# Optimization experiments

Hardware: AMD Instinct MI355X
Metric: run time of the kernel (lower is better)

The kernel has to match this reference:

```python
import jax, jax.numpy as jnp
import numpy as np

D = 384      # embedding_dim (module-level global)
H = 6        # num_heads
HD = D // H  # head_size = 64
T = 256      # block_size (tril buffer cap)
B = 128


def _layernorm(x, gamma, beta, eps=1e-5):
    mu = jnp.mean(x, axis=-1, keepdims=True)
    var = jnp.var(x, axis=-1, keepdims=True)
    return (x - mu) * jax.lax.rsqrt(var + eps) * gamma + beta


def setup_inputs() -> dict:
    key = jax.random.key(0)
    ks = jax.random.split(key, 12)
    s = 0.02
    return {
        "x":   jax.random.normal(ks[0], (B, T, D), jnp.float32),
        "Wq":  jax.random.normal(ks[1], (H, D, HD), jnp.float32) * s,
        "Wk":  jax.random.normal(ks[2], (H, D, HD), jnp.float32) * s,
        "Wv":  jax.random.normal(ks[3], (H, D, HD), jnp.float32) * s,
        "Wp":  jax.random.normal(ks[4], (D, D), jnp.float32) * s,
        "bp":  jnp.zeros((D,), jnp.float32),
        "W1":  jax.random.normal(ks[5], (D, 4 * D), jnp.float32) * s,
        "b1":  jnp.zeros((4 * D,), jnp.float32),
        "W2":  jax.random.normal(ks[6], (4 * D, D), jnp.float32) * s,
        "b2":  jnp.zeros((D,), jnp.float32),
        "g1":  jnp.ones((D,), jnp.float32),
        "be1": jnp.zeros((D,), jnp.float32),
        "g2":  jnp.ones((D,), jnp.float32),
        "be2": jnp.zeros((D,), jnp.float32),
    }


def reference(x, Wq, Wk, Wv, Wp, bp, W1, b1, W2, b2, g1, be1, g2, be2):
    Bsz, Tlen, C = x.shape
    # pre-LN self-attention
    h = _layernorm(x, g1, be1)
    q = jnp.einsum("btd,hdk->bhtk", h, Wq)
    k = jnp.einsum("bsd,hdk->bhsk", h, Wk)
    v = jnp.einsum("bsd,hdk->bhsk", h, Wv)
    # NOTE: source divides by sqrt(C)=sqrt(embedding_dim), not sqrt(head_size)
    scores = jnp.einsum("bhtk,bhsk->bhts", q, k) / jnp.sqrt(jnp.float32(C))
    causal = jnp.tril(jnp.ones((Tlen, Tlen), bool))
    scores = jnp.where(causal, scores, jnp.float32(-jnp.inf))
    attn = jax.nn.softmax(scores, axis=-1)          # dropout = identity (eval)
    o = jnp.einsum("bhts,bhsk->bhtk", attn, v)      # [B,H,T,HD]
    o = o.transpose(0, 2, 1, 3).reshape(Bsz, Tlen, C)  # concat heads
    sa = o @ Wp + bp
    x = x + sa
    # pre-LN feed-forward
    h2 = _layernorm(x, g2, be2)
    ff = jax.nn.relu(h2 @ W1 + b1) @ W2 + b2
    return x + ff
```

## Files before the change

kernel.cpp:

```cpp
#include <hip/hip_runtime.h>
#include <cstdint>
#include <cstddef>

#define D_   384
#define Hn   6
#define HDm  64
#define T_   256
#define B_   128
#define NROW (B_ * T_)

typedef __bf16  bf16x8 __attribute__((ext_vector_type(8)));
typedef float   f32x4  __attribute__((ext_vector_type(4)));
typedef const __attribute__((address_space(1))) void gvoid;
typedef __attribute__((address_space(3))) void lvoid;

__device__ inline uint32_t bf16rn(float f) {
  uint32_t u = __float_as_uint(f);
  return (u + 0x7FFFu + ((u >> 16) & 1u)) >> 16;
}

__global__ __launch_bounds__(128) void ln_kernel(const float* __restrict__ x,
                                                 const float* __restrict__ g,
                                                 const float* __restrict__ b,
                                                 uint16_t* __restrict__ out) {
  int row = blockIdx.x, tid = threadIdx.x;
  const float* xr = x + (size_t)row * D_;
  float v0 = xr[tid], v1 = xr[tid + 128], v2 = xr[tid + 256];
  float s  = v0 + v1 + v2;
  float ss = v0 * v0 + v1 * v1 + v2 * v2;
#pragma unroll
  for (int off = 32; off > 0; off >>= 1) {
    s  += __shfl_down(s, off);
    ss += __shfl_down(ss, off);
  }
  __shared__ float red[4];
  if ((tid & 63) == 0) { red[(tid >> 6) * 2] = s; red[(tid >> 6) * 2 + 1] = ss; }
  __syncthreads();
  float S = red[0] + red[2], SS = red[1] + red[3];
  float mu  = S * (1.0f / D_);
  float var = SS * (1.0f / D_) - mu * mu;
  float inv = rsqrtf(var + 1e-5f);
  uint16_t* orow = out + (size_t)row * D_;
  orow[tid]       = (uint16_t)bf16rn((v0 - mu) * inv * g[tid]       + b[tid]);
  orow[tid + 128] = (uint16_t)bf16rn((v1 - mu) * inv * g[tid + 128] + b[tid + 128]);
  orow[tid + 256] = (uint16_t)bf16rn((v2 - mu) * inv * g[tid + 256] + b[tid + 256]);
}

__global__ __launch_bounds__(256) void pack_qkv_w(const float* __restrict__ Wq,
                                                  const float* __restrict__ Wk,
                                                  const float* __restrict__ Wv,
                                                  uint16_t* __restrict__ Wo) {
  int idx = blockIdx.x * 256 + threadIdx.x;
  if (idx >= 1152 * D_) return;
  int col = idx / D_, d = idx % D_;
  int which = col / 384, c2 = col % 384;
  int h = c2 / HDm, k = c2 % HDm;
  const float* W = (which == 0) ? Wq : (which == 1) ? Wk : Wv;
  Wo[idx] = (uint16_t)bf16rn(W[((size_t)h * D_ + d) * HDm + k]);
}

__global__ __launch_bounds__(256) void pack_wt(const float* __restrict__ W,
                                               uint16_t* __restrict__ Wt,
                                               int K, int N) {
  int idx = blockIdx.x * 256 + threadIdx.x;
  if (idx >= K * N) return;
  int n = idx / K, k = idx % K;
  Wt[idx] = (uint16_t)bf16rn(W[(size_t)k * N + n]);
}

__global__ __launch_bounds__(256) void gemm_bf16(const uint16_t* __restrict__ A,
                                                 const uint16_t* __restrict__ Bt,
                                                 const float* __restrict__ bias,
                                                 const float* __restrict__ resid,
                                                 void* __restrict__ Cout,
                                                 int M, int N, int K,
                                                 int relu, int store_f32) {
  __shared__ uint16_t As[128 * 32];
  __shared__ uint16_t Bs[128 * 32];
  int tid = threadIdx.x;
  int bm = blockIdx.x * 128, bn = blockIdx.y * 128;
  int lane = tid & 63, wave = tid >> 6;
  int wm = (wave >> 1) << 6;
  int wn = (wave & 1) << 6;
  int lr = lane & 15;
  int q  = lane >> 4;
  int r0 = q << 2;
  int rd_off = (q ^ (lr & 3)) << 3;

  f32x4 acc[4][4];
  const f32x4 zero = {0.f, 0.f, 0.f, 0.f};
#pragma unroll
  for (int i = 0; i < 4; ++i)
#pragma unroll
    for (int j = 0; j < 4; ++j) acc[i][j] = zero;

  for (int k0 = 0; k0 < K; k0 += 32) {
    __syncthreads();
#pragma unroll
    for (int t = 0; t < 2; ++t) {
      int c = t * 256 + tid;
      int row = c >> 2, cc = c & 3;
      int gc = cc ^ (row & 3);
      const uint16_t* ga = A  + (size_t)(bm + row) * K + (k0 + gc * 8);
      const uint16_t* gb = Bt + (size_t)(bn + row) * K + (k0 + gc * 8);
      __builtin_amdgcn_global_load_lds((gvoid*)ga, (lvoid*)((char*)As + c * 16), 16, 0, 0);
      __builtin_amdgcn_global_load_lds((gvoid*)gb, (lvoid*)((char*)Bs + c * 16), 16, 0, 0);
    }
    __syncthreads();

    bf16x8 af[4], bfr[4];
#pragma unroll
    for (int i = 0; i < 4; ++i)
      af[i] = *(const bf16x8*)&As[(wm + i * 16 + lr) * 32 + rd_off];
#pragma unroll
    for (int j = 0; j < 4; ++j)
      bfr[j] = *(const bf16x8*)&Bs[(wn + j * 16 + lr) * 32 + rd_off];
#pragma unroll
    for (int i = 0; i < 4; ++i)
#pragma unroll
      for (int j = 0; j < 4; ++j)
        acc[i][j] = __builtin_amdgcn_mfma_f32_16x16x32_bf16(af[i], bfr[j], acc[i][j], 0, 0, 0);
  }

#pragma unroll
  for (int i = 0; i < 4; ++i) {
#pragma unroll
    for (int r = 0; r < 4; ++r) {
      int rr = bm + wm + i * 16 + r0 + r;
#pragma unroll
      for (int j = 0; j < 4; ++j) {
        int col = bn + wn + j * 16 + lr;
        float v = acc[i][j][r];
        if (bias)  v += bias[col];
        if (relu)  v = fmaxf(v, 0.0f);
        if (resid) v += resid[(size_t)rr * N + col];
        if (store_f32) ((float*)Cout)[(size_t)rr * N + col] = v;
        else           ((uint16_t*)Cout)[(size_t)rr * N + col] = (uint16_t)bf16rn(v);
      }
    }
  }
}

__global__ __launch_bounds__(256, 2) void attn_mfma(const uint16_t* __restrict__ qkv,
                                                    uint16_t* __restrict__ o) {
  __shared__ uint16_t Kt[64 * 72];
  __shared__ uint16_t Vt[64 * 72];
  __shared__ uint16_t Pb[4 * 64 * 72];
  int bh = blockIdx.x;
  int b = bh / Hn, h = bh % Hn;
  int tid = threadIdx.x;
  int lane = tid & 63, w = tid >> 6;
  int ln = lane & 15, q = lane >> 4;
  int kq = q * 8;
  int m0 = w * 64;
  const uint16_t* base = qkv + (size_t)b * T_ * 1152;

  bf16x8 af[4][2];
#pragma unroll
  for (int i = 0; i < 4; ++i)
#pragma unroll
    for (int ks = 0; ks < 2; ++ks)
      af[i][ks] = *(const bf16x8*)(base + (size_t)(m0 + i * 16 + ln) * 1152 + h * HDm + ks * 32 + kq);

  f32x4 o_[4][4], m_[4], l_[4];
  const f32x4 zero = {0.f, 0.f, 0.f, 0.f};
#pragma unroll
  for (int i = 0; i < 4; ++i) {
    m_[i] = {-1e30f, -1e30f, -1e30f, -1e30f};
    l_[i] = zero;
#pragma unroll
    for (int n = 0; n < 4; ++n) o_[i][n] = zero;
  }
  const float cs = 0.07362222f;

  for (int jt = 0; jt < 4; ++jt) {
    if (jt) __syncthreads();
#pragma unroll
    for (int t = 0; t < 2; ++t) {
      int c = t * 256 + tid;
      int s = c >> 3, d0 = (c & 7) << 3;
      *(uint4*)&Kt[s * 72 + d0] =
          *(const uint4*)(base + (size_t)(jt * 64 + s) * 1152 + 384 + h * HDm + d0);
    }
    {
      int sv = tid & 63, dv = (tid >> 6) << 4;
      const uint16_t* gv = base + (size_t)(jt * 64 + sv) * 1152 + 768 + h * HDm + dv;
      uint16_t tmp[16];
      *(uint4*)&tmp[0] = *(const uint4*)gv;
      *(uint4*)&tmp[8] = *(const uint4*)(gv + 8);
#pragma unroll
      for (int jj = 0; jj < 16; ++jj) Vt[(dv + jj) * 72 + sv] = tmp[jj];
    }
    __syncthreads();

    if (w >= jt) {
      f32x4 s2[4][4];
#pragma unroll
      for (int i = 0; i < 4; ++i)
#pragma unroll
        for (int j = 0; j < 4; ++j) s2[i][j] = zero;
#pragma unroll
      for (int ks = 0; ks < 2; ++ks) {
        bf16x8 bf[4];
#pragma unroll
        for (int j = 0; j < 4; ++j)
          bf[j] = *(const bf16x8*)&Kt[(j * 16 + ln) * 72 + ks * 32 + kq];
#pragma unroll
        for (int i = 0; i < 4; ++i)
#pragma unroll
          for (int j = 0; j < 4; ++j)
            s2[i][j] = __builtin_amdgcn_mfma_f32_16x16x32_bf16(af[i][ks], bf[j], s2[i][j], 0, 0, 0);
      }
#pragma unroll
      for (int i = 0; i < 4; ++i) {
#pragma unroll
        for (int j = 0; j < 4; ++j)
#pragma unroll
          for (int r = 0; r < 4; ++r) s2[i][j][r] *= cs;
        if (jt == w) {
#pragma unroll
          for (int j = 0; j < 4; ++j)
#pragma unroll
            for (int r = 0; r < 4; ++r)
              if (j * 16 + ln > i * 16 + q * 4 + r) s2[i][j][r] = -1e30f;
        }
        f32x4 rm;
#pragma unroll
        for (int r = 0; r < 4; ++r)
          rm[r] = fmaxf(fmaxf(s2[i][0][r], s2[i][1][r]), fmaxf(s2[i][2][r], s2[i][3][r]));
#pragma unroll
        for (int off = 1; off < 16; off <<= 1)
#pragma unroll
          for (int r = 0; r < 4; ++r)
            rm[r] = fmaxf(rm[r], __shfl_xor(rm[r], off));
        f32x4 mn, al, ps;
#pragma unroll
        for (int r = 0; r < 4; ++r) {
          mn[r] = fmaxf(m_[i][r], rm[r]);
          al[r] = exp2f(m_[i][r] - mn[r]);
          ps[r] = 0.f;
        }
        m_[i] = mn;
#pragma unroll
        for (int j = 0; j < 4; ++j)
#pragma unroll
          for (int r = 0; r < 4; ++r) {
            float p = exp2f(s2[i][j][r] - mn[r]);
            s2[i][j][r] = p;
            ps[r] += p;
          }
#pragma unroll
        for (int r = 0; r < 4; ++r) l_[i][r] = l_[i][r] * al[r] + ps[r];
#pragma unroll
        for (int n = 0; n < 4; ++n)
#pragma unroll
          for (int r = 0; r < 4; ++r) o_[i][n][r] *= al[r];
#pragma unroll
        for (int j = 0; j < 4; ++j)
#pragma unroll
          for (int r = 0; r < 4; ++r)
            Pb[w * 4608 + (i * 16 + q * 4 + r) * 72 + j * 16 + ln] =
                (uint16_t)bf16rn(s2[i][j][r]);
      }
      bf16x8 pa[4][2];
#pragma unroll
      for (int i = 0; i < 4; ++i)
#pragma unroll
        for (int ks = 0; ks < 2; ++ks)
          pa[i][ks] = *(const bf16x8*)&Pb[w * 4608 + (i * 16 + ln) * 72 + ks * 32 + kq];
#pragma unroll
      for (int n = 0; n < 4; ++n) {
        bf16x8 bv0 = *(const bf16x8*)&Vt[(n * 16 + ln) * 72 + kq];
        bf16x8 bv1 = *(const bf16x8*)&Vt[(n * 16 + ln) * 72 + 32 + kq];
#pragma unroll
        for (int i = 0; i < 4; ++i) {
          o_[i][n] = __builtin_amdgcn_mfma_f32_16x16x32_bf16(pa[i][0], bv0, o_[i][n], 0, 0, 0);
          o_[i][n] = __builtin_amdgcn_mfma_f32_16x16x32_bf16(pa[i][1], bv1, o_[i][n], 0, 0, 0);
        }
      }
    }
  }
#pragma unroll
  for (int i = 0; i < 4; ++i) {
    f32x4 lt = l_[i];
#pragma unroll
    for (int off = 1; off < 16; off <<= 1)
#pragma unroll
      for (int r = 0; r < 4; ++r) lt[r] += __shfl_xor(lt[r], off);
#pragma unroll
    for (int r = 0; r < 4; ++r) {
      float inv = 1.0f / lt[r];
      int row = b * T_ + m0 + i * 16 + q * 4 + r;
      uint16_t* op = o + (size_t)row * D_ + h * HDm;
#pragma unroll
      for (int n = 0; n < 4; ++n)
        op[n * 16 + ln] = (uint16_t)bf16rn(o_[i][n][r] * inv);
    }
  }
}

extern "C" void kernel_launch(void* const* d_in, const int* in_sizes, int n_in,
                              void* d_out, int out_size, void* d_ws, size_t ws_size,
                              hipStream_t stream) {
  const float* x   = (const float*)d_in[0];
  const float* Wq  = (const float*)d_in[1];
  const float* Wk  = (const float*)d_in[2];
  const float* Wv  = (const float*)d_in[3];
  const float* Wp  = (const float*)d_in[4];
  const float* bp  = (const float*)d_in[5];
  const float* W1  = (const float*)d_in[6];
  const float* b1  = (const float*)d_in[7];
  const float* W2  = (const float*)d_in[8];
  const float* b2  = (const float*)d_in[9];
  const float* g1  = (const float*)d_in[10];
  const float* be1 = (const float*)d_in[11];
  const float* g2  = (const float*)d_in[12];
  const float* be2 = (const float*)d_in[13];
  float* out = (float*)d_out;

  char* ws = (char*)d_ws;
  uint16_t* hbuf  = (uint16_t*)ws;
  uint16_t* qkv   = (uint16_t*)(ws + 25165824ull);
  uint16_t* ob    = (uint16_t*)(ws + 100663296ull);
  uint16_t* ff1   = qkv;
  uint16_t* Wqkvt = (uint16_t*)(ws + 125829120ull);
  uint16_t* Wpt   = (uint16_t*)(ws + 126713856ull);
  uint16_t* W1t   = (uint16_t*)(ws + 127008768ull);
  uint16_t* W2t   = (uint16_t*)(ws + 128188416ull);

  pack_qkv_w<<<(1152 * D_ + 255) / 256, 256, 0, stream>>>(Wq, Wk, Wv, Wqkvt);
  pack_wt<<<(384 * 384 + 255) / 256, 256, 0, stream>>>(Wp, Wpt, 384, 384);
  pack_wt<<<(384 * 1536 + 255) / 256, 256, 0, stream>>>(W1, W1t, 384, 1536);
  pack_wt<<<(1536 * 384 + 255) / 256, 256, 0, stream>>>(W2, W2t, 1536, 384);
  ln_kernel<<<NROW, 128, 0, stream>>>(x, g1, be1, hbuf);
  gemm_bf16<<<dim3(NROW / 128, 1152 / 128), 256, 0, stream>>>(
      hbuf, Wqkvt, nullptr, nullptr, qkv, NROW, 1152, 384, 0, 0);
  attn_mfma<<<B_ * Hn, 256, 0, stream>>>(qkv, ob);
  gemm_bf16<<<dim3(NROW / 128, 384 / 128), 256, 0, stream>>>(
      ob, Wpt, bp, x, out, NROW, 384, 384, 0, 1);
  ln_kernel<<<NROW, 128, 0, stream>>>(out, g2, be2, hbuf);
  gemm_bf16<<<dim3(NROW / 128, 1536 / 128), 256, 0, stream>>>(
      hbuf, W1t, b1, nullptr, ff1, NROW, 1536, 384, 1, 0);
  gemm_bf16<<<dim3(NROW / 128, 384 / 128), 256, 0, stream>>>(
      ff1, W2t, b2, out, out, NROW, 384, 1536, 0, 1);
}
```

Measured before the change: 540.6 us.

## Double-buffer LDS tiles in bf16 GEMM to overlap global loads with MFMA

```diff
diff --git a/kernel.cpp b/kernel.cpp
--- a/kernel.cpp
+++ b/kernel.cpp
@@ -75,8 +75,8 @@
                                                  void* __restrict__ Cout,
                                                  int M, int N, int K,
                                                  int relu, int store_f32) {
-  __shared__ uint16_t As[128 * 32];
-  __shared__ uint16_t Bs[128 * 32];
+  __shared__ uint16_t As[2][128 * 32];
+  __shared__ uint16_t Bs[2][128 * 32];
   int tid = threadIdx.x;
   int bm = blockIdx.x * 128, bn = blockIdx.y * 128;
   int lane = tid & 63, wave = tid >> 6;
@@ -87,6 +87,15 @@
   int r0 = q << 2;
   int rd_off = (q ^ (lr & 3)) << 3;
 
+  int c0 = tid,        row0 = c0 >> 2;
+  int c1 = 256 + tid,  row1 = c1 >> 2;
+  int g0 = ((c0 & 3) ^ (row0 & 3)) << 3;
+  int g1 = ((c1 & 3) ^ (row1 & 3)) << 3;
+  const uint16_t* ga0 = A  + (size_t)(bm + row0) * K + g0;
+  const uint16_t* ga1 = A  + (size_t)(bm + row1) * K + g1;
+  const uint16_t* gb0 = Bt + (size_t)(bn + row0) * K + g0;
+  const uint16_t* gb1 = Bt + (size_t)(bn + row1) * K + g1;
+
   f32x4 acc[4][4];
   const f32x4 zero = {0.f, 0.f, 0.f, 0.f};
 #pragma unroll
@@ -94,32 +103,35 @@
 #pragma unroll
     for (int j = 0; j < 4; ++j) acc[i][j] = zero;
 
-  for (int k0 = 0; k0 < K; k0 += 32) {
+  int nk = K >> 5;
+  __builtin_amdgcn_global_load_lds((gvoid*)ga0, (lvoid*)((char*)As[0] + c0 * 16), 16, 0, 0);
+  __builtin_amdgcn_global_load_lds((gvoid*)gb0, (lvoid*)((char*)Bs[0] + c0 * 16), 16, 0, 0);
+  __builtin_amdgcn_global_load_lds((gvoid*)ga1, (lvoid*)((char*)As[0] + c1 * 16), 16, 0, 0);
+  __builtin_amdgcn_global_load_lds((gvoid*)gb1, (lvoid*)((char*)Bs[0] + c1 * 16), 16, 0, 0);
+
+  for (int i = 0; i < nk; ++i) {
+    int cur = i & 1;
     __syncthreads();
-#pragma unroll
-    for (int t = 0; t < 2; ++t) {
-      int c = t * 256 + tid;
-      int row = c >> 2, cc = c & 3;
-      int gc = cc ^ (row & 3);
-      const uint16_t* ga = A  + (size_t)(bm + row) * K + (k0 + gc * 8);
-      const uint16_t* gb = Bt + (size_t)(bn + row) * K + (k0 + gc * 8);
-      __builtin_amdgcn_global_load_lds((gvoid*)ga, (lvoid*)((char*)As + c * 16), 16, 0, 0);
-      __builtin_amdgcn_global_load_lds((gvoid*)gb, (lvoid*)((char*)Bs + c * 16), 16, 0, 0);
-    }
-    __syncthreads();
+    if (i + 1 < nk) {
+      int nxt = cur ^ 1, ko = (i + 1) << 5;
+      __builtin_amdgcn_global_load_lds((gvoid*)(ga0 + ko), (lvoid*)((char*)As[nxt] + c0 * 16), 16, 0, 0);
+      __builtin_amdgcn_global_load_lds((gvoid*)(gb0 + ko), (lvoid*)((char*)Bs[nxt] + c0 * 16), 16, 0, 0);
+      __builtin_amdgcn_global_load_lds((gvoid*)(ga1 + ko), (lvoid*)((char*)As[nxt] + c1 * 16), 16, 0, 0);
+      __builtin_amdgcn_global_load_lds((gvoid*)(gb1 + ko), (lvoid*)((char*)Bs[nxt] + c1 * 16), 16, 0, 0);
+    }
 
     bf16x8 af[4], bfr[4];
 #pragma unroll
-    for (int i = 0; i < 4; ++i)
-      af[i] = *(const bf16x8*)&As[(wm + i * 16 + lr) * 32 + rd_off];
+    for (int ii = 0; ii < 4; ++ii)
+      af[ii] = *(const bf16x8*)&As[cur][(wm + ii * 16 + lr) * 32 + rd_off];
 #pragma unroll
     for (int j = 0; j < 4; ++j)
-      bfr[j] = *(const bf16x8*)&Bs[(wn + j * 16 + lr) * 32 + rd_off];
-#pragma unroll
-    for (int i = 0; i < 4; ++i)
+      bfr[j] = *(const bf16x8*)&Bs[cur][(wn + j * 16 + lr) * 32 + rd_off];
+#pragma unroll
+    for (int ii = 0; ii < 4; ++ii)
 #pragma unroll
       for (int j = 0; j < 4; ++j)
-        acc[i][j] = __builtin_amdgcn_mfma_f32_16x16x32_bf16(af[i], bfr[j], acc[i][j], 0, 0, 0);
+        acc[ii][j] = __builtin_amdgcn_mfma_f32_16x16x32_bf16(af[ii], bfr[j], acc[ii][j], 0, 0, 0);
   }
 
 #pragma unroll
```

After: 520.2 us. 1.04x faster.
